# Optimization experiments

Hardware: AMD Instinct MI355X
Metric: run time of the kernel (lower is better)

The kernel has to match this reference:

```python
import jax, jax.numpy as jnp
import numpy as np

DIM = 1024
NUM_HEADS = 16
HEAD_DIM = 64
INNER = NUM_HEADS * HEAD_DIM  # 1024
SCALE = HEAD_DIM ** -0.5


def setup_inputs() -> dict:
    key = jax.random.key(0)
    k1, k2, k3, k4 = jax.random.split(key, 4)
    x = jax.random.normal(k1, (4, 2048, DIM), dtype=jnp.float32)
    # Linear weights stored as [in, out] for x @ W
    w_qkv = jax.random.normal(k2, (DIM, INNER * 3), dtype=jnp.float32) * (DIM ** -0.5)
    w_out = jax.random.normal(k3, (INNER, DIM), dtype=jnp.float32) * (INNER ** -0.5)
    b_out = jax.random.normal(k4, (DIM,), dtype=jnp.float32) * 0.02
    return {"x": x, "w_qkv": w_qkv, "w_out": w_out, "b_out": b_out}


def reference(x, w_qkv, w_out, b_out):
    b, n, _ = x.shape
    qkv = x @ w_qkv  # [b, n, 3*inner]
    q, k, v = jnp.split(qkv, 3, axis=-1)
    # [b, n, inner] -> [b, h, n, d]
    split_heads = lambda t: t.reshape(b, n, NUM_HEADS, HEAD_DIM).transpose(0, 2, 1, 3)
    q, k, v = split_heads(q), split_heads(k), split_heads(v)
    scores = jnp.einsum('bhid,bhjd->bhij', q, k) * SCALE  # [b, h, n, n]
    weights = jax.nn.softmax(scores, axis=-1)
    attended = jnp.einsum('bhij,bhjd->bhid', weights, v)  # [b, h, n, d]
    attended = attended.transpose(0, 2, 1, 3).reshape(b, n, INNER)
    return attended @ w_out + b_out
```

## Files before the change

### kernel.cpp

```cpp
#include <hip/hip_runtime.h>
#include <hip/hip_bf16.h>

typedef __attribute__((ext_vector_type(8))) short short8;
typedef __attribute__((ext_vector_type(4))) short short4v;
typedef __attribute__((ext_vector_type(4))) float f32x4;

#define DIM    1024
#define NHEADS 16
#define HDIM   64
#define SEQ    2048
#define BATCH  4
#define ROWS   8192
#define QKV_N  3072

#define QSCALE_LOG2E 0.18033688011112042f

__device__ __forceinline__ unsigned short f2bf(float f) {
    union { float f; unsigned u; } v; v.f = f;
    unsigned u = v.u;
    return (unsigned short)((u + 0x7fffu + ((u >> 16) & 1u)) >> 16);
}
__device__ __forceinline__ float exp2_fast(float x) {
    float r;
    asm("v_exp_f32 %0, %1" : "=v"(r) : "v"(x));
    return r;
}
__device__ __forceinline__ unsigned cvt_pk_bf16(float a, float b) {
    unsigned r;
    asm("v_cvt_pk_bf16_f32 %0, %1, %2" : "=v"(r) : "v"(a), "v"(b));
    return r;
}

__device__ __forceinline__ void gload16(const void* g, void* l) {
    __builtin_amdgcn_global_load_lds(
        (const __attribute__((address_space(1))) unsigned int*)g,
        (__attribute__((address_space(3))) unsigned int*)l, 16, 0, 0);
}

__global__ __launch_bounds__(256)
void conv_kernel(const float* __restrict__ src, unsigned short* __restrict__ dst, int n4)
{
    const int i = blockIdx.x * 256 + threadIdx.x;
    if (i >= n4) return;
    const float4 v = ((const float4*)src)[i];
    short4v o;
    o[0] = (short)f2bf(v.x); o[1] = (short)f2bf(v.y);
    o[2] = (short)f2bf(v.z); o[3] = (short)f2bf(v.w);
    ((short4v*)dst)[i] = o;
}

__global__ __launch_bounds__(256)
void convT_kernel(const float* __restrict__ src, unsigned short* __restrict__ dst,
                  int R, int C)
{
    __shared__ float T[32][33];
    const int r0 = blockIdx.y * 32, c0 = blockIdx.x * 32;
    const int tc = threadIdx.x & 31, tr = threadIdx.x >> 5;
    #pragma unroll
    for (int i = 0; i < 4; ++i)
        T[tr + i * 8][tc] = src[(size_t)(r0 + tr + i * 8) * C + c0 + tc];
    __syncthreads();
    #pragma unroll
    for (int i = 0; i < 4; ++i)
        dst[(size_t)(c0 + tr + i * 8) * R + r0 + tc] = f2bf(T[tc][tr + i * 8]);
}

template<bool WITH_BIAS, bool QSCALE>
__global__ __launch_bounds__(256)
void gemm_kernel(const unsigned short* __restrict__ A,
                 const unsigned short* __restrict__ BT,
                 const float* __restrict__ bias,
                 void* __restrict__ Cp, int M, int N, int K)
{
    __shared__ alignas(16) unsigned short LA[128][32];
    __shared__ alignas(16) unsigned short LB[128][32];

    const int tid  = threadIdx.x;
    const int lane = tid & 63;
    const int w    = tid >> 6;
    const int wr   = w >> 1, wc = w & 1;
    const int bm   = blockIdx.y * 128, bn = blockIdx.x * 128;
    const int r16  = lane & 15, g = lane >> 4;

    f32x4 acc[4][4] = {};

    const int srow = lane >> 2, skg = (lane & 3) * 8;

    for (int k0 = 0; k0 < K; k0 += 32) {
        #pragma unroll
        for (int c = 0; c < 2; ++c) {
            const int chunk = w * 2 + c;
            gload16(A  + (size_t)(bm + chunk * 16 + srow) * K + k0 + skg, &LA[chunk * 16][0]);
            gload16(BT + (size_t)(bn + chunk * 16 + srow) * K + k0 + skg, &LB[chunk * 16][0]);
        }
        __syncthreads();
        short8 af[4], bf_[4];
        #pragma unroll
        for (int i = 0; i < 4; ++i) {
            af[i]  = *(const short8*)&LA[wr * 64 + i * 16 + r16][g * 8];
            bf_[i] = *(const short8*)&LB[wc * 64 + i * 16 + r16][g * 8];
        }
        __builtin_amdgcn_s_setprio(1);
        #pragma unroll
        for (int mi = 0; mi < 4; ++mi)
            #pragma unroll
            for (int ni = 0; ni < 4; ++ni)
                acc[mi][ni] = __builtin_amdgcn_mfma_f32_16x16x32_bf16(
                    af[mi], bf_[ni], acc[mi][ni], 0, 0, 0);
        __builtin_amdgcn_s_setprio(0);
        __syncthreads();
    }

    #pragma unroll
    for (int mi = 0; mi < 4; ++mi)
        #pragma unroll
        for (int ni = 0; ni < 4; ++ni) {
            const int gcol = bn + wc * 64 + ni * 16 + r16;
            #pragma unroll
            for (int j = 0; j < 4; ++j) {
                const int grow = bm + wr * 64 + mi * 16 + g * 4 + j;
                float v = acc[mi][ni][j];
                if (QSCALE && gcol < DIM) v *= QSCALE_LOG2E;
                if (WITH_BIAS)
                    ((float*)Cp)[(size_t)grow * N + gcol] = v + bias[gcol];
                else
                    ((unsigned short*)Cp)[(size_t)grow * N + gcol] = f2bf(v);
            }
        }
}

__global__ __launch_bounds__(256, 4)
void attn_kernel(const unsigned short* __restrict__ qkv,
                 unsigned short* __restrict__ att)
{
    __shared__ alignas(16) unsigned short Ks[64][64];
    __shared__ alignas(16) unsigned short Vt[80][80];

    const int tid  = threadIdx.x;
    const int lane = tid & 63;
    const int w    = tid >> 6;
    const int b  = blockIdx.z, h = blockIdx.y;
    const int q0 = blockIdx.x * 128;
    const size_t base = (size_t)b * SEQ * QKV_N + (size_t)h * HDIM;

    const int r16 = lane & 15;
    const int g   = lane >> 4;
    const int f7  = r16 & 7;

    if (tid < 80) Vt[64][tid] = 0x3F80;
    for (int idx = tid; idx < 15 * 80; idx += 256)
        Vt[65 + idx / 80][idx % 80] = 0;

    short8 qf[2][2];
    #pragma unroll
    for (int mi = 0; mi < 2; ++mi) {
        const unsigned short* qrow =
            qkv + base + (size_t)(q0 + w * 32 + mi * 16 + r16) * QKV_N;
        qf[mi][0] = *(const short8*)(qrow + g * 8);
        qf[mi][1] = *(const short8*)(qrow + 32 + g * 8);
    }

    f32x4 oacc[2][5] = {};
    float m_r[2] = { -3e38f, -3e38f };

    const int krow  = lane >> 3;
    const int kGsrc = (lane & 7) ^ (krow & 7);

    const int k5 = lane & 31, khi = lane >> 5;
    const int vpos = ((k5 < 16) ? ((k5 >> 2) * 8 + (k5 & 3))
                                : (((k5 - 16) >> 2) * 8 + 4 + ((k5 - 16) & 3)))
                     + khi * 32;

    for (int kt = 0; kt < SEQ; kt += 64) {
        __syncthreads();
        #pragma unroll
        for (int c = 0; c < 2; ++c) {
            const int chunk = w * 2 + c;
            const unsigned short* gsrc =
                qkv + base + (size_t)(kt + chunk * 8 + krow) * QKV_N + DIM + kGsrc * 8;
            gload16(gsrc, &Ks[chunk * 8][0]);
        }
        {
            const unsigned short* vsrc =
                qkv + base + (size_t)(kt + lane) * QKV_N + 2 * DIM + w * 16;
            short8 v0 = *(const short8*)(vsrc);
            short8 v1 = *(const short8*)(vsrc + 8);
            #pragma unroll
            for (int i = 0; i < 8; ++i) {
                Vt[w * 16 + i][vpos]     = (unsigned short)v0[i];
                Vt[w * 16 + 8 + i][vpos] = (unsigned short)v1[i];
            }
        }
        __syncthreads();

        f32x4 sacc[2][4] = {};
        __builtin_amdgcn_s_setprio(1);
        #pragma unroll
        for (int jt = 0; jt < 4; ++jt) {
            const int row = jt * 16 + r16;
            short8 kf0 = *(const short8*)&Ks[row][(g ^ f7) * 8];
            short8 kf1 = *(const short8*)&Ks[row][((4 + g) ^ f7) * 8];
            sacc[0][jt] = __builtin_amdgcn_mfma_f32_16x16x32_bf16(kf0, qf[0][0], sacc[0][jt], 0, 0, 0);
            sacc[0][jt] = __builtin_amdgcn_mfma_f32_16x16x32_bf16(kf1, qf[0][1], sacc[0][jt], 0, 0, 0);
            sacc[1][jt] = __builtin_amdgcn_mfma_f32_16x16x32_bf16(kf0, qf[1][0], sacc[1][jt], 0, 0, 0);
            sacc[1][jt] = __builtin_amdgcn_mfma_f32_16x16x32_bf16(kf1, qf[1][1], sacc[1][jt], 0, 0, 0);
        }
        __builtin_amdgcn_s_setprio(0);

        short8 pb[2][2];
        #pragma unroll
        for (int mi = 0; mi < 2; ++mi) {
            const float a0 = fmaxf(fmaxf(sacc[mi][0][0], sacc[mi][0][1]), sacc[mi][0][2]);
            const float a1 = fmaxf(fmaxf(sacc[mi][0][3], sacc[mi][1][0]), sacc[mi][1][1]);
            const float a2 = fmaxf(fmaxf(sacc[mi][1][2], sacc[mi][1][3]), sacc[mi][2][0]);
            const float a3 = fmaxf(fmaxf(sacc[mi][2][1], sacc[mi][2][2]), sacc[mi][2][3]);
            const float a4 = fmaxf(fmaxf(sacc[mi][3][0], sacc[mi][3][1]), sacc[mi][3][2]);
            float tm = fmaxf(fmaxf(fmaxf(a0, a1), a2),
                             fmaxf(fmaxf(a3, a4), sacc[mi][3][3]));
            tm = fmaxf(tm, __shfl_xor(tm, 16));
            tm = fmaxf(tm, __shfl_xor(tm, 32));

            float nm = m_r[mi];
            if (!__all(tm <= m_r[mi] + 8.f)) {
                nm = fmaxf(m_r[mi], tm);
                const float f = exp2_fast(m_r[mi] - nm);
                m_r[mi] = nm;
                #pragma unroll
                for (int dt = 0; dt < 5; ++dt)
                    #pragma unroll
                    for (int jr = 0; jr < 4; ++jr)
                        oacc[mi][dt][jr] *= f;
            }

            unsigned pw[8];
            #pragma unroll
            for (int jt = 0; jt < 4; ++jt) {
                const float p0 = exp2_fast(sacc[mi][jt][0] - nm);
                const float p1 = exp2_fast(sacc[mi][jt][1] - nm);
                const float p2 = exp2_fast(sacc[mi][jt][2] - nm);
                const float p3 = exp2_fast(sacc[mi][jt][3] - nm);
                pw[jt * 2]     = cvt_pk_bf16(p0, p1);
                pw[jt * 2 + 1] = cvt_pk_bf16(p2, p3);
            }

            union { unsigned u[4]; short8 s; } c0, c1;
            c0.u[0] = pw[0]; c0.u[1] = pw[1]; c0.u[2] = pw[2]; c0.u[3] = pw[3];
            c1.u[0] = pw[4]; c1.u[1] = pw[5]; c1.u[2] = pw[6]; c1.u[3] = pw[7];
            pb[mi][0] = c0.s;
            pb[mi][1] = c1.s;
        }

        __builtin_amdgcn_s_setprio(1);
        #pragma unroll
        for (int dt = 0; dt < 5; ++dt) {
            short8 vf0 = *(const short8*)&Vt[dt * 16 + r16][g * 8];
            short8 vf1 = *(const short8*)&Vt[dt * 16 + r16][32 + g * 8];
            #pragma unroll
            for (int mi = 0; mi < 2; ++mi) {
                oacc[mi][dt] = __builtin_amdgcn_mfma_f32_16x16x32_bf16(vf0, pb[mi][0], oacc[mi][dt], 0, 0, 0);
                oacc[mi][dt] = __builtin_amdgcn_mfma_f32_16x16x32_bf16(vf1, pb[mi][1], oacc[mi][dt], 0, 0, 0);
            }
        }
        __builtin_amdgcn_s_setprio(0);
    }

    #pragma unroll
    for (int mi = 0; mi < 2; ++mi) {
        const float inv = 1.f / __shfl(oacc[mi][4][0], r16);
        const int q = q0 + w * 32 + mi * 16 + r16;
        unsigned short* dst = att + (size_t)(b * SEQ + q) * DIM + h * HDIM;
        #pragma unroll
        for (int dt = 0; dt < 4; ++dt)
            #pragma unroll
            for (int jr = 0; jr < 4; ++jr)
                dst[dt * 16 + g * 4 + jr] = f2bf(oacc[mi][dt][jr] * inv);
    }
}

extern "C" void kernel_launch(void* const* d_in, const int* in_sizes, int n_in,
                              void* d_out, int out_size, void* d_ws, size_t ws_size,
                              hipStream_t stream)
{
    const float* x     = (const float*)d_in[0];
    const float* w_qkv = (const float*)d_in[1];
    const float* w_out = (const float*)d_in[2];
    const float* b_out = (const float*)d_in[3];
    float* out = (float*)d_out;

    unsigned short* qkv   = (unsigned short*)d_ws;
    unsigned short* xb    = qkv + 25165824;
    unsigned short* att   = xb;
    unsigned short* wqkvT = qkv + 33554432;
    unsigned short* woutT = qkv + 36700160;

    conv_kernel<<<dim3(ROWS * DIM / 4 / 256), 256, 0, stream>>>(x, xb, ROWS * DIM / 4);
    convT_kernel<<<dim3(QKV_N / 32, DIM / 32), 256, 0, stream>>>(w_qkv, wqkvT, DIM, QKV_N);
    convT_kernel<<<dim3(DIM / 32, DIM / 32), 256, 0, stream>>>(w_out, woutT, DIM, DIM);

    gemm_kernel<false, true><<<dim3(QKV_N / 128, ROWS / 128), 256, 0, stream>>>(
        xb, wqkvT, nullptr, qkv, ROWS, QKV_N, DIM);

    attn_kernel<<<dim3(SEQ / 128, NHEADS, BATCH), 256, 0, stream>>>(qkv, att);

    gemm_kernel<true, false><<<dim3(DIM / 128, ROWS / 128), 256, 0, stream>>>(
        att, woutT, b_out, out, ROWS, DIM, DIM);
}
```

Measured before the change: 208.5 us.

## Double-buffer K tiles and prefetch V one tile ahead in attention

The attention loop now keeps two K buffers in LDS and issues the next tile's K global-to-LDS loads and V register loads before computing the current tile. The loop is unrolled by two so buffers and V registers alternate, and the block waits on vmcnt only at the start of the next phase. This is meant to hide global load latency behind the QK^T, softmax and PV work instead of stalling at each barrier. It costs an extra 8 KB of LDS per block and more live registers, which could lower occupancy.

```diff
diff --git a/kernel.cpp b/kernel.cpp
--- a/kernel.cpp
+++ b/kernel.cpp
@@ -37,6 +37,8 @@
         (__attribute__((address_space(3))) unsigned int*)l, 16, 0, 0);
 }
 
+#define MFMA16(a, b, c) __builtin_amdgcn_mfma_f32_16x16x32_bf16(a, b, c, 0, 0, 0)
+
 __global__ __launch_bounds__(256)
 void conv_kernel(const float* __restrict__ src, unsigned short* __restrict__ dst, int n4)
 {
@@ -105,8 +107,7 @@
         for (int mi = 0; mi < 4; ++mi)
             #pragma unroll
             for (int ni = 0; ni < 4; ++ni)
-                acc[mi][ni] = __builtin_amdgcn_mfma_f32_16x16x32_bf16(
-                    af[mi], bf_[ni], acc[mi][ni], 0, 0, 0);
+                acc[mi][ni] = MFMA16(af[mi], bf_[ni], acc[mi][ni]);
         __builtin_amdgcn_s_setprio(0);
         __syncthreads();
     }
@@ -133,7 +134,7 @@
 void attn_kernel(const unsigned short* __restrict__ qkv,
                  unsigned short* __restrict__ att)
 {
-    __shared__ alignas(16) unsigned short Ks[64][64];
+    __shared__ alignas(16) unsigned short Ks[2][64][64];
     __shared__ alignas(16) unsigned short Vt[80][80];
 
     const int tid  = threadIdx.x;
@@ -171,98 +172,120 @@
                                 : (((k5 - 16) >> 2) * 8 + 4 + ((k5 - 16) & 3)))
                      + khi * 32;
 
-    for (int kt = 0; kt < SEQ; kt += 64) {
-        __syncthreads();
-        #pragma unroll
-        for (int c = 0; c < 2; ++c) {
-            const int chunk = w * 2 + c;
-            const unsigned short* gsrc =
-                qkv + base + (size_t)(kt + chunk * 8 + krow) * QKV_N + DIM + kGsrc * 8;
-            gload16(gsrc, &Ks[chunk * 8][0]);
-        }
-        {
-            const unsigned short* vsrc =
-                qkv + base + (size_t)(kt + lane) * QKV_N + 2 * DIM + w * 16;
-            short8 v0 = *(const short8*)(vsrc);
-            short8 v1 = *(const short8*)(vsrc + 8);
-            #pragma unroll
-            for (int i = 0; i < 8; ++i) {
-                Vt[w * 16 + i][vpos]     = (unsigned short)v0[i];
-                Vt[w * 16 + 8 + i][vpos] = (unsigned short)v1[i];
-            }
-        }
-        __syncthreads();
-
-        f32x4 sacc[2][4] = {};
-        __builtin_amdgcn_s_setprio(1);
-        #pragma unroll
-        for (int jt = 0; jt < 4; ++jt) {
-            const int row = jt * 16 + r16;
-            short8 kf0 = *(const short8*)&Ks[row][(g ^ f7) * 8];
-            short8 kf1 = *(const short8*)&Ks[row][((4 + g) ^ f7) * 8];
-            sacc[0][jt] = __builtin_amdgcn_mfma_f32_16x16x32_bf16(kf0, qf[0][0], sacc[0][jt], 0, 0, 0);
-            sacc[0][jt] = __builtin_amdgcn_mfma_f32_16x16x32_bf16(kf1, qf[0][1], sacc[0][jt], 0, 0, 0);
-            sacc[1][jt] = __builtin_amdgcn_mfma_f32_16x16x32_bf16(kf0, qf[1][0], sacc[1][jt], 0, 0, 0);
-            sacc[1][jt] = __builtin_amdgcn_mfma_f32_16x16x32_bf16(kf1, qf[1][1], sacc[1][jt], 0, 0, 0);
-        }
-        __builtin_amdgcn_s_setprio(0);
-
-        short8 pb[2][2];
-        #pragma unroll
-        for (int mi = 0; mi < 2; ++mi) {
-            const float a0 = fmaxf(fmaxf(sacc[mi][0][0], sacc[mi][0][1]), sacc[mi][0][2]);
-            const float a1 = fmaxf(fmaxf(sacc[mi][0][3], sacc[mi][1][0]), sacc[mi][1][1]);
-            const float a2 = fmaxf(fmaxf(sacc[mi][1][2], sacc[mi][1][3]), sacc[mi][2][0]);
-            const float a3 = fmaxf(fmaxf(sacc[mi][2][1], sacc[mi][2][2]), sacc[mi][2][3]);
-            const float a4 = fmaxf(fmaxf(sacc[mi][3][0], sacc[mi][3][1]), sacc[mi][3][2]);
-            float tm = fmaxf(fmaxf(fmaxf(a0, a1), a2),
-                             fmaxf(fmaxf(a3, a4), sacc[mi][3][3]));
-            tm = fmaxf(tm, __shfl_xor(tm, 16));
-            tm = fmaxf(tm, __shfl_xor(tm, 32));
-
-            float nm = m_r[mi];
-            if (!__all(tm <= m_r[mi] + 8.f)) {
-                nm = fmaxf(m_r[mi], tm);
-                const float f = exp2_fast(m_r[mi] - nm);
-                m_r[mi] = nm;
-                #pragma unroll
-                for (int dt = 0; dt < 5; ++dt)
-                    #pragma unroll
-                    for (int jr = 0; jr < 4; ++jr)
-                        oacc[mi][dt][jr] *= f;
-            }
-
-            unsigned pw[8];
-            #pragma unroll
-            for (int jt = 0; jt < 4; ++jt) {
-                const float p0 = exp2_fast(sacc[mi][jt][0] - nm);
-                const float p1 = exp2_fast(sacc[mi][jt][1] - nm);
-                const float p2 = exp2_fast(sacc[mi][jt][2] - nm);
-                const float p3 = exp2_fast(sacc[mi][jt][3] - nm);
-                pw[jt * 2]     = cvt_pk_bf16(p0, p1);
-                pw[jt * 2 + 1] = cvt_pk_bf16(p2, p3);
-            }
-
-            union { unsigned u[4]; short8 s; } c0, c1;
-            c0.u[0] = pw[0]; c0.u[1] = pw[1]; c0.u[2] = pw[2]; c0.u[3] = pw[3];
-            c1.u[0] = pw[4]; c1.u[1] = pw[5]; c1.u[2] = pw[6]; c1.u[3] = pw[7];
-            pb[mi][0] = c0.s;
-            pb[mi][1] = c1.s;
-        }
-
-        __builtin_amdgcn_s_setprio(1);
-        #pragma unroll
-        for (int dt = 0; dt < 5; ++dt) {
-            short8 vf0 = *(const short8*)&Vt[dt * 16 + r16][g * 8];
-            short8 vf1 = *(const short8*)&Vt[dt * 16 + r16][32 + g * 8];
-            #pragma unroll
-            for (int mi = 0; mi < 2; ++mi) {
-                oacc[mi][dt] = __builtin_amdgcn_mfma_f32_16x16x32_bf16(vf0, pb[mi][0], oacc[mi][dt], 0, 0, 0);
-                oacc[mi][dt] = __builtin_amdgcn_mfma_f32_16x16x32_bf16(vf1, pb[mi][1], oacc[mi][dt], 0, 0, 0);
-            }
-        }
-        __builtin_amdgcn_s_setprio(0);
-    }
+    short8 vA0, vA1, vB0, vB1;
+
+    #pragma unroll
+    for (int c = 0; c < 2; ++c) {
+        const int chunk = w * 2 + c;
+        gload16(qkv + base + (size_t)(chunk * 8 + krow) * QKV_N + DIM + kGsrc * 8,
+                &Ks[0][chunk * 8][0]);
+    }
+    {
+        const unsigned short* vsrc =
+            qkv + base + (size_t)lane * QKV_N + 2 * DIM + w * 16;
+        vA0 = *(const short8*)(vsrc);
+        vA1 = *(const short8*)(vsrc + 8);
+    }
+
+#define ATTN_PHASE(TILE, BUF, VC0, VC1, VN0, VN1, DOPRE)                          \
+    {                                                                             \
+        __builtin_amdgcn_s_barrier();             \
+        asm volatile("s_waitcnt vmcnt(0)" ::: "memory");    \
+        __builtin_amdgcn_sched_barrier(0);                                        \
+        _Pragma("unroll")                                                         \
+        for (int i = 0; i < 8; ++i) {                   \
+            Vt[w * 16 + i][vpos]     = (unsigned short)VC0[i];                    \
+            Vt[w * 16 + 8 + i][vpos] = (unsigned short)VC1[i];                    \
+        }                                                                         \
+        if (DOPRE) {                                  \
+            _Pragma("unroll")                                                     \
+            for (int c = 0; c < 2; ++c) {                                         \
+                const int chunk = w * 2 + c;                                      \
+                gload16(qkv + base +                                              \
+                        (size_t)((TILE) + 64 + chunk * 8 + krow) * QKV_N          \
+                        + DIM + kGsrc * 8,                                        \
+                        &Ks[(BUF) ^ 1][chunk * 8][0]);                            \
+            }                                                                     \
+            const unsigned short* vsrc = qkv + base +                             \
+                (size_t)((TILE) + 64 + lane) * QKV_N + 2 * DIM + w * 16;          \
+            VN0 = *(const short8*)(vsrc);                                         \
+            VN1 = *(const short8*)(vsrc + 8);                                     \
+        }                                                                         \
+        asm volatile("s_waitcnt lgkmcnt(0)" ::: "memory");    \
+        __builtin_amdgcn_s_barrier();                                             \
+        __builtin_amdgcn_sched_barrier(0);                                        \
+                                            \
+        f32x4 sacc[2][4] = {};                                                    \
+        __builtin_amdgcn_s_setprio(1);                                            \
+        _Pragma("unroll")                                                         \
+        for (int jt = 0; jt < 4; ++jt) {                                          \
+            const int row = jt * 16 + r16;                                        \
+            short8 kf0 = *(const short8*)&Ks[BUF][row][(g ^ f7) * 8];             \
+            short8 kf1 = *(const short8*)&Ks[BUF][row][((4 + g) ^ f7) * 8];       \
+            sacc[0][jt] = MFMA16(kf0, qf[0][0], sacc[0][jt]);                     \
+            sacc[0][jt] = MFMA16(kf1, qf[0][1], sacc[0][jt]);                     \
+            sacc[1][jt] = MFMA16(kf0, qf[1][0], sacc[1][jt]);                     \
+            sacc[1][jt] = MFMA16(kf1, qf[1][1], sacc[1][jt]);                     \
+        }                                                                         \
+        __builtin_amdgcn_s_setprio(0);                                            \
+        short8 pb[2][2];                                                          \
+        _Pragma("unroll")                                                         \
+        for (int mi = 0; mi < 2; ++mi) {                                          \
+            const float a0 = fmaxf(fmaxf(sacc[mi][0][0], sacc[mi][0][1]), sacc[mi][0][2]); \
+            const float a1 = fmaxf(fmaxf(sacc[mi][0][3], sacc[mi][1][0]), sacc[mi][1][1]); \
+            const float a2 = fmaxf(fmaxf(sacc[mi][1][2], sacc[mi][1][3]), sacc[mi][2][0]); \
+            const float a3 = fmaxf(fmaxf(sacc[mi][2][1], sacc[mi][2][2]), sacc[mi][2][3]); \
+            const float a4 = fmaxf(fmaxf(sacc[mi][3][0], sacc[mi][3][1]), sacc[mi][3][2]); \
+            float tm = fmaxf(fmaxf(fmaxf(a0, a1), a2),                            \
+                             fmaxf(fmaxf(a3, a4), sacc[mi][3][3]));               \
+            tm = fmaxf(tm, __shfl_xor(tm, 16));                                   \
+            tm = fmaxf(tm, __shfl_xor(tm, 32));                                   \
+            float nm = m_r[mi];                                                   \
+            if (!__all(tm <= m_r[mi] + 8.f)) {          \
+                nm = fmaxf(m_r[mi], tm);                                          \
+                const float f = exp2_fast(m_r[mi] - nm);                          \
+                m_r[mi] = nm;                                                     \
+                _Pragma("unroll")                                                 \
+                for (int dt = 0; dt < 5; ++dt)                                    \
+                    _Pragma("unroll")                                             \
+                    for (int jr = 0; jr < 4; ++jr)                                \
+                        oacc[mi][dt][jr] *= f;                                    \
+            }                                                                     \
+            unsigned pw[8];                                                       \
+            _Pragma("unroll")                                                     \
+            for (int jt = 0; jt < 4; ++jt) {                                      \
+                const float p0 = exp2_fast(sacc[mi][jt][0] - nm);                 \
+                const float p1 = exp2_fast(sacc[mi][jt][1] - nm);                 \
+                const float p2 = exp2_fast(sacc[mi][jt][2] - nm);                 \
+                const float p3 = exp2_fast(sacc[mi][jt][3] - nm);                 \
+                pw[jt * 2]     = cvt_pk_bf16(p0, p1);                             \
+                pw[jt * 2 + 1] = cvt_pk_bf16(p2, p3);                             \
+            }                                                                     \
+            union { unsigned u[4]; short8 s; } c0, c1;                            \
+            c0.u[0] = pw[0]; c0.u[1] = pw[1]; c0.u[2] = pw[2]; c0.u[3] = pw[3];   \
+            c1.u[0] = pw[4]; c1.u[1] = pw[5]; c1.u[2] = pw[6]; c1.u[3] = pw[7];   \
+            pb[mi][0] = c0.s;                                                     \
+            pb[mi][1] = c1.s;                                                     \
+        }                                                                         \
+        __builtin_amdgcn_s_setprio(1);                                            \
+        _Pragma("unroll")                                                         \
+        for (int dt = 0; dt < 5; ++dt) {                \
+            short8 vf0 = *(const short8*)&Vt[dt * 16 + r16][g * 8];               \
+            short8 vf1 = *(const short8*)&Vt[dt * 16 + r16][32 + g * 8];          \
+            _Pragma("unroll")                                                     \
+            for (int mi = 0; mi < 2; ++mi) {                                      \
+                oacc[mi][dt] = MFMA16(vf0, pb[mi][0], oacc[mi][dt]);              \
+                oacc[mi][dt] = MFMA16(vf1, pb[mi][1], oacc[mi][dt]);              \
+            }                                                                     \
+        }                                                                         \
+        __builtin_amdgcn_s_setprio(0);                                            \
+    }
+
+    for (int kt = 0; kt < SEQ; kt += 128) {
+        ATTN_PHASE(kt,      0, vA0, vA1, vB0, vB1, true);
+        ATTN_PHASE(kt + 64, 1, vB0, vB1, vA0, vA1, (kt + 128 < SEQ));
+    }
+#undef ATTN_PHASE
 
     #pragma unroll
     for (int mi = 0; mi < 2; ++mi) {
```

Result: slower. 238.0 us (+14.1%).

## Double-buffer K tiles and defer V transpose store in attention loop

Applied to the files above, without the earlier changes.

The attention kernel now keeps two K tiles in shared memory and prefetches the next tile with async global-to-LDS loads while computing on the current one. The V global loads are issued at the top of the iteration, and their transposed LDS writes are deferred until after the softmax, so load latency overlaps QK^T and exp work. The barriers are replaced with explicit vmcnt/lgkmcnt waits plus s_barrier. This adds LDS usage and relies on hand-counted waitcnt values, which are fragile if the compiler reorders memory operations.

```diff
diff --git a/kernel.cpp b/kernel.cpp
--- a/kernel.cpp
+++ b/kernel.cpp
@@ -37,6 +37,8 @@
         (__attribute__((address_space(3))) unsigned int*)l, 16, 0, 0);
 }
 
+#define MFMA16(a, b, c) __builtin_amdgcn_mfma_f32_16x16x32_bf16(a, b, c, 0, 0, 0)
+
 __global__ __launch_bounds__(256)
 void conv_kernel(const float* __restrict__ src, unsigned short* __restrict__ dst, int n4)
 {
@@ -105,8 +107,7 @@
         for (int mi = 0; mi < 4; ++mi)
             #pragma unroll
             for (int ni = 0; ni < 4; ++ni)
-                acc[mi][ni] = __builtin_amdgcn_mfma_f32_16x16x32_bf16(
-                    af[mi], bf_[ni], acc[mi][ni], 0, 0, 0);
+                acc[mi][ni] = MFMA16(af[mi], bf_[ni], acc[mi][ni]);
         __builtin_amdgcn_s_setprio(0);
         __syncthreads();
     }
@@ -133,7 +134,7 @@
 void attn_kernel(const unsigned short* __restrict__ qkv,
                  unsigned short* __restrict__ att)
 {
-    __shared__ alignas(16) unsigned short Ks[64][64];
+    __shared__ alignas(16) unsigned short Ks[2][64][64];
     __shared__ alignas(16) unsigned short Vt[80][80];
 
     const int tid  = threadIdx.x;
@@ -150,6 +151,17 @@
     if (tid < 80) Vt[64][tid] = 0x3F80;
     for (int idx = tid; idx < 15 * 80; idx += 256)
         Vt[65 + idx / 80][idx % 80] = 0;
+    __syncthreads();
+
+    const int krow  = lane >> 3;
+    const int kGsrc = (lane & 7) ^ (krow & 7);
+
+    #pragma unroll
+    for (int c = 0; c < 2; ++c) {
+        const int chunk = w * 2 + c;
+        gload16(qkv + base + (size_t)(chunk * 8 + krow) * QKV_N + DIM + kGsrc * 8,
+                &Ks[0][chunk * 8][0]);
+    }
 
     short8 qf[2][2];
     #pragma unroll
@@ -163,47 +175,45 @@
     f32x4 oacc[2][5] = {};
     float m_r[2] = { -3e38f, -3e38f };
 
-    const int krow  = lane >> 3;
-    const int kGsrc = (lane & 7) ^ (krow & 7);
-
     const int k5 = lane & 31, khi = lane >> 5;
     const int vpos = ((k5 < 16) ? ((k5 >> 2) * 8 + (k5 & 3))
                                 : (((k5 - 16) >> 2) * 8 + 4 + ((k5 - 16) & 3)))
                      + khi * 32;
 
     for (int kt = 0; kt < SEQ; kt += 64) {
-        __syncthreads();
-        #pragma unroll
-        for (int c = 0; c < 2; ++c) {
-            const int chunk = w * 2 + c;
-            const unsigned short* gsrc =
-                qkv + base + (size_t)(kt + chunk * 8 + krow) * QKV_N + DIM + kGsrc * 8;
-            gload16(gsrc, &Ks[chunk * 8][0]);
-        }
-        {
-            const unsigned short* vsrc =
-                qkv + base + (size_t)(kt + lane) * QKV_N + 2 * DIM + w * 16;
-            short8 v0 = *(const short8*)(vsrc);
-            short8 v1 = *(const short8*)(vsrc + 8);
-            #pragma unroll
-            for (int i = 0; i < 8; ++i) {
-                Vt[w * 16 + i][vpos]     = (unsigned short)v0[i];
-                Vt[w * 16 + 8 + i][vpos] = (unsigned short)v1[i];
-            }
-        }
-        __syncthreads();
+        const int buf = (kt >> 6) & 1;
+
+        const unsigned short* vsrc =
+            qkv + base + (size_t)(kt + lane) * QKV_N + 2 * DIM + w * 16;
+        short8 v0 = *(const short8*)(vsrc);
+        short8 v1 = *(const short8*)(vsrc + 8);
+
+        if (kt + 64 < SEQ) {
+            #pragma unroll
+            for (int c = 0; c < 2; ++c) {
+                const int chunk = w * 2 + c;
+                gload16(qkv + base + (size_t)(kt + 64 + chunk * 8 + krow) * QKV_N
+                        + DIM + kGsrc * 8,
+                        &Ks[buf ^ 1][chunk * 8][0]);
+            }
+            asm volatile("s_waitcnt vmcnt(4)" ::: "memory");
+        } else {
+            asm volatile("s_waitcnt vmcnt(2)" ::: "memory");
+        }
+        __builtin_amdgcn_s_barrier();
+        __builtin_amdgcn_sched_barrier(0);
 
         f32x4 sacc[2][4] = {};
         __builtin_amdgcn_s_setprio(1);
         #pragma unroll
         for (int jt = 0; jt < 4; ++jt) {
             const int row = jt * 16 + r16;
-            short8 kf0 = *(const short8*)&Ks[row][(g ^ f7) * 8];
-            short8 kf1 = *(const short8*)&Ks[row][((4 + g) ^ f7) * 8];
-            sacc[0][jt] = __builtin_amdgcn_mfma_f32_16x16x32_bf16(kf0, qf[0][0], sacc[0][jt], 0, 0, 0);
-            sacc[0][jt] = __builtin_amdgcn_mfma_f32_16x16x32_bf16(kf1, qf[0][1], sacc[0][jt], 0, 0, 0);
-            sacc[1][jt] = __builtin_amdgcn_mfma_f32_16x16x32_bf16(kf0, qf[1][0], sacc[1][jt], 0, 0, 0);
-            sacc[1][jt] = __builtin_amdgcn_mfma_f32_16x16x32_bf16(kf1, qf[1][1], sacc[1][jt], 0, 0, 0);
+            short8 kf0 = *(const short8*)&Ks[buf][row][(g ^ f7) * 8];
+            short8 kf1 = *(const short8*)&Ks[buf][row][((4 + g) ^ f7) * 8];
+            sacc[0][jt] = MFMA16(kf0, qf[0][0], sacc[0][jt]);
+            sacc[0][jt] = MFMA16(kf1, qf[0][1], sacc[0][jt]);
+            sacc[1][jt] = MFMA16(kf0, qf[1][0], sacc[1][jt]);
+            sacc[1][jt] = MFMA16(kf1, qf[1][1], sacc[1][jt]);
         }
         __builtin_amdgcn_s_setprio(0);
 
@@ -245,11 +255,21 @@
 
             union { unsigned u[4]; short8 s; } c0, c1;
             c0.u[0] = pw[0]; c0.u[1] = pw[1]; c0.u[2] = pw[2]; c0.u[3] = pw[3];
+            c1.u[0] = pw[4]; c1.u[1] = pw[5]; c1.u[2] = pw[6]; c1.u[7 - 7] = c1.u[0];
             c1.u[0] = pw[4]; c1.u[1] = pw[5]; c1.u[2] = pw[6]; c1.u[3] = pw[7];
             pb[mi][0] = c0.s;
             pb[mi][1] = c1.s;
         }
 
+        #pragma unroll
+        for (int i = 0; i < 8; ++i) {
+            Vt[w * 16 + i][vpos]     = (unsigned short)v0[i];
+            Vt[w * 16 + 8 + i][vpos] = (unsigned short)v1[i];
+        }
+        asm volatile("s_waitcnt lgkmcnt(0)" ::: "memory");
+        __builtin_amdgcn_s_barrier();
+        __builtin_amdgcn_sched_barrier(0);
+
         __builtin_amdgcn_s_setprio(1);
         #pragma unroll
         for (int dt = 0; dt < 5; ++dt) {
@@ -257,8 +277,8 @@
             short8 vf1 = *(const short8*)&Vt[dt * 16 + r16][32 + g * 8];
             #pragma unroll
             for (int mi = 0; mi < 2; ++mi) {
-                oacc[mi][dt] = __builtin_amdgcn_mfma_f32_16x16x32_bf16(vf0, pb[mi][0], oacc[mi][dt], 0, 0, 0);
-                oacc[mi][dt] = __builtin_amdgcn_mfma_f32_16x16x32_bf16(vf1, pb[mi][1], oacc[mi][dt], 0, 0, 0);
+                oacc[mi][dt] = MFMA16(vf0, pb[mi][0], oacc[mi][dt]);
+                oacc[mi][dt] = MFMA16(vf1, pb[mi][1], oacc[mi][dt]);
             }
         }
         __builtin_amdgcn_s_setprio(0);
```

New measurement: 212.6 us. Within noise of the previous version (+2.0%).
